# Performance work log

Hardware: AMD Instinct MI355X
Metric: run time of the kernel (lower is better)

## Reference

```python
import jax, jax.numpy as jnp
import numpy as np

B, S, E, H, M, Q = 2, 2048, 768, 12, 768, 4
D = E // H  # head_dim = 64
EPS = 1e-5


def _layernorm(x, g, b):
    m = jnp.mean(x, axis=-1, keepdims=True)
    v = jnp.mean((x - m) ** 2, axis=-1, keepdims=True)
    return (x - m) / jnp.sqrt(v + EPS) * g + b


def setup_inputs() -> dict:
    key = jax.random.key(0)
    ks = jax.random.split(key, 12)
    w = lambda k, shape, s=0.02: (jax.random.normal(k, shape) * s).astype(jnp.float32)
    return {
        "x": jax.random.normal(ks[0], (B, S, E), dtype=jnp.float32),
        "ln1_g": jnp.ones((E,), jnp.float32), "ln1_b": jnp.zeros((E,), jnp.float32),
        "wq": w(ks[1], (E, E)), "bq": jnp.zeros((E,), jnp.float32),
        "wk": w(ks[2], (E, E)), "bk": jnp.zeros((E,), jnp.float32),
        "wv": w(ks[3], (E, E)), "bv": jnp.zeros((E,), jnp.float32),
        "wo": w(ks[4], (E, E)), "bo": jnp.zeros((E,), jnp.float32),
        "ln2_g": jnp.ones((E,), jnp.float32), "ln2_b": jnp.zeros((E,), jnp.float32),
        "w1": w(ks[5], (E, Q * M)), "b1": jnp.zeros((Q * M,), jnp.float32),
        "wvqc": w(ks[6], (M, M)), "bvqc": jnp.zeros((M,), jnp.float32),
        "w2": w(ks[7], (Q * M, E)), "b2": jnp.zeros((E,), jnp.float32),
    }


def reference(x, ln1_g, ln1_b, wq, bq, wk, bk, wv, bv, wo, bo,
              ln2_g, ln2_b, w1, b1, wvqc, bvqc, w2, b2):
    b, s, e = x.shape
    h, d = H, e // H

    # --- attention branch (pre-norm, per-query-L2-normalized logits) ---
    xn = _layernorm(x, ln1_g, ln1_b)
    q = (xn @ wq + bq).reshape(b, s, h, d).transpose(0, 2, 1, 3)  # bhsd
    k = (xn @ wk + bk).reshape(b, s, h, d).transpose(0, 2, 1, 3)
    v = (xn @ wv + bv).reshape(b, s, h, d).transpose(0, 2, 1, 3)

    qk = jnp.einsum('bhsd,bhtd->bhst', q, k)                       # [B,H,S,S]
    q_norm2 = jnp.clip(jnp.sum(q * q, axis=-1, keepdims=True), 1e-5)  # [B,H,S,1]
    logits = qk / jnp.sqrt(d * q_norm2)
    attn = jax.nn.softmax(logits, axis=-1)
    vals = jnp.einsum('bhst,bhtd->bhsd', attn, v)
    vals = vals.transpose(0, 2, 1, 3).reshape(b, s, e)
    x = x + (vals @ wo + bo)  # residual; attn dropout is identity in eval

    # --- quantum-style FeedForward with overlapping q_stride slices ---
    xn2 = _layernorm(x, ln2_g, ln2_b)
    hmid = xn2 @ w1 + b1                                           # [B,S,Q*M]
    m = wvqc.shape[0]
    qstride = w1.shape[1] // m
    # overlapping slices h[..., i:i+M] for i in 0..Q-1, stacked on a new axis
    sl = jnp.stack([hmid[..., i:i + m] for i in range(qstride)], axis=2)  # [B,S,Q,M]
    hv = sl @ wvqc + bvqc                                          # vqc linear
    hv = hv.transpose(0, 1, 3, 2).reshape(b, s, qstride * m)       # interleave
    hv = jax.nn.gelu(hv, approximate=False)
    out = x + (hv @ w2 + b2)
    return out
```

## Files before the change

kernel.cpp:

```cpp
#include <hip/hip_runtime.h>
#include <hip/hip_bf16.h>
#include <math.h>

typedef unsigned short ushort_t;
typedef __attribute__((ext_vector_type(8))) short short8;
typedef __attribute__((ext_vector_type(8))) __bf16 bf16x8;
typedef __attribute__((ext_vector_type(4))) float f32x4;
typedef __attribute__((ext_vector_type(4))) unsigned u32x4;

#define SDIM 2048
#define EDIM 768
#define NTOK 4096

static __device__ __forceinline__ ushort_t f2bf(float f) {
  unsigned u = __builtin_bit_cast(unsigned, f);
  u += 0x7fff + ((u >> 16) & 1);
  return (ushort_t)(u >> 16);
}
static __device__ __forceinline__ float bf2f(ushort_t h) {
  return __builtin_bit_cast(float, (unsigned)h << 16);
}
static __device__ __forceinline__ f32x4 mfma16(short8 a, short8 b, f32x4 c) {
  return __builtin_amdgcn_mfma_f32_16x16x32_bf16(
      __builtin_bit_cast(bf16x8, a), __builtin_bit_cast(bf16x8, b), c, 0, 0, 0);
}
static __device__ __forceinline__ void gload_lds16(const void* g, void* l) {
  __builtin_amdgcn_global_load_lds(
      (const __attribute__((address_space(1))) void*)g,
      (__attribute__((address_space(3))) void*)l, 16, 0, 0);
}
static __device__ __forceinline__ unsigned cvtpk(float lo, float hi) {
  unsigned r;
  asm("v_cvt_pk_bf16_f32 %0, %1, %2" : "=v"(r) : "v"(lo), "v"(hi));
  return r;
}
static __device__ __forceinline__ float exp2fast(float x) {
  float r;
  asm("v_exp_f32 %0, %1" : "=v"(r) : "v"(x));
  return r;
}

__global__ void k_castT5(const float* __restrict__ wq, const float* __restrict__ wk,
                         const float* __restrict__ wv, const float* __restrict__ wo,
                         const float* __restrict__ wvqc, ushort_t* __restrict__ oqkv,
                         ushort_t* __restrict__ owo, ushort_t* __restrict__ ovqc) {
  __shared__ float tile[32][33];
  const int z = blockIdx.z;
  const float* in = z == 0 ? wq : z == 1 ? wk : z == 2 ? wv : z == 3 ? wo : wvqc;
  ushort_t* out = z < 3 ? oqkv + (size_t)z * 768 * 768 : (z == 3 ? owo : ovqc);
  int c0 = blockIdx.x * 32, r0 = blockIdx.y * 32;
  int tx = threadIdx.x, ty = threadIdx.y;
#pragma unroll
  for (int i = 0; i < 32; i += 8)
    tile[ty + i][tx] = in[(size_t)(r0 + ty + i) * 768 + c0 + tx];
  __syncthreads();
#pragma unroll
  for (int i = 0; i < 32; i += 8)
    out[(size_t)(c0 + ty + i) * 768 + r0 + tx] = f2bf(tile[tx][ty + i]);
}

__global__ void k_castT(const float* __restrict__ in, ushort_t* __restrict__ out,
                        int R, int C) {
  __shared__ float tile[32][33];
  int c0 = blockIdx.x * 32, r0 = blockIdx.y * 32;
  int tx = threadIdx.x, ty = threadIdx.y;
#pragma unroll
  for (int i = 0; i < 32; i += 8)
    tile[ty + i][tx] = in[(size_t)(r0 + ty + i) * C + c0 + tx];
  __syncthreads();
#pragma unroll
  for (int i = 0; i < 32; i += 8)
    out[(size_t)(c0 + ty + i) * R + r0 + tx] = f2bf(tile[tx][ty + i]);
}

__global__ void k_vT(const ushort_t* __restrict__ in, ushort_t* __restrict__ out) {
  __shared__ ushort_t tile[32][34];
  int bh = blockIdx.z;
  int t0 = blockIdx.x * 32, d0 = blockIdx.y * 32;
  const ushort_t* ib = in + (size_t)bh * SDIM * 64;
  ushort_t* ob = out + (size_t)bh * 64 * SDIM;
  int tx = threadIdx.x, ty = threadIdx.y;
#pragma unroll
  for (int i = 0; i < 32; i += 8)
    tile[ty + i][tx] = ib[(size_t)(t0 + ty + i) * 64 + d0 + tx];
  __syncthreads();
  const int T = t0 + tx, tb = T & ~63, tl = T & 63;
  const int tperm =
      tb + 32 * (tl >> 5) + 8 * ((tl >> 2) & 3) + 4 * ((tl >> 4) & 1) + (tl & 3);
#pragma unroll
  for (int i = 0; i < 32; i += 8)
    ob[(size_t)(d0 + ty + i) * SDIM + tperm] = tile[tx][ty + i];
}

__global__ void k_w1shift(const float* __restrict__ w1, ushort_t* __restrict__ w1s) {
  int idx = blockIdx.x * 256 + threadIdx.x;
  int e = idx / 768, m = idx - (idx / 768) * 768;
#pragma unroll
  for (int i = 0; i < 4; i++)
    w1s[((size_t)i * 768 + e) * 768 + m] = f2bf(w1[(size_t)e * 3072 + i + m]);
}

__global__ __launch_bounds__(256) void k_b1eff(const float* __restrict__ b1,
                                               const ushort_t* __restrict__ wvqcT,
                                               const float* __restrict__ bvqc,
                                               float* __restrict__ b1e) {
  const int n = blockIdx.x;
  const int i = n & 3, j = n >> 2;
  const int t = threadIdx.x;
  float s = 0.f;
  for (int m = t; m < 768; m += 256)
    s += b1[i + m] * bf2f(wvqcT[(size_t)j * 768 + m]);
#pragma unroll
  for (int mm = 32; mm; mm >>= 1) s += __shfl_xor(s, mm);
  __shared__ float red[4];
  if ((t & 63) == 0) red[t >> 6] = s;
  __syncthreads();
  if (t == 0) b1e[n] = red[0] + red[1] + red[2] + red[3] + bvqc[j];
}

__global__ __launch_bounds__(256) void k_ln(const float* __restrict__ x,
                                            const float* __restrict__ gam,
                                            const float* __restrict__ bet,
                                            ushort_t* __restrict__ out) {
  const int row = blockIdx.x, t = threadIdx.x;
  const float* xr = x + (size_t)row * EDIM;
  float v0 = xr[t], v1 = xr[t + 256], v2 = xr[t + 512];
  float s = v0 + v1 + v2;
  float s2 = v0 * v0 + v1 * v1 + v2 * v2;
#pragma unroll
  for (int m = 32; m; m >>= 1) { s += __shfl_xor(s, m); s2 += __shfl_xor(s2, m); }
  __shared__ float red[8];
  const int wid = t >> 6, lane = t & 63;
  if (lane == 0) { red[wid] = s; red[4 + wid] = s2; }
  __syncthreads();
  s = red[0] + red[1] + red[2] + red[3];
  s2 = red[4] + red[5] + red[6] + red[7];
  float mean = s * (1.f / EDIM);
  float var = s2 * (1.f / EDIM) - mean * mean;
  float rstd = rsqrtf(var + 1e-5f);
  ushort_t* orow = out + (size_t)row * EDIM;
  orow[t] = f2bf((v0 - mean) * rstd * gam[t] + bet[t]);
  orow[t + 256] = f2bf((v1 - mean) * rstd * gam[t + 256] + bet[t + 256]);
  orow[t + 512] = f2bf((v2 - mean) * rstd * gam[t + 512] + bet[t + 512]);
}

__global__ __launch_bounds__(256) void k_qscale(const ushort_t* __restrict__ q,
                                                float* __restrict__ qs) {
  const int lane = threadIdx.x & 63, w = threadIdx.x >> 6;
  const int row = blockIdx.x * 4 + w;
  float v = bf2f(q[(size_t)row * 64 + lane]);
  float s = v * v;
#pragma unroll
  for (int m = 32; m; m >>= 1) s += __shfl_xor(s, m);
  if (lane == 0) qs[row] = rsqrtf(64.f * fmaxf(s, 1e-5f));
}

template <int MODE, int BM, int BN, int BK>
__global__ __launch_bounds__(256) void k_gemm(
    const ushort_t* __restrict__ A, const ushort_t* __restrict__ Bt, int lda,
    int ldb, int kc, const float* __restrict__ b0, const float* __restrict__ b1p,
    const float* __restrict__ b2p, float* __restrict__ outF,
    const float* __restrict__ resid, ushort_t* __restrict__ o0,
    ushort_t* __restrict__ o1, ushort_t* __restrict__ o2, int ldc) {
  constexpr int MT = BM / 32, NT = BN / 32;
  constexpr int KCH = BK / 8;
  constexpr int NPA = BM * BK / 2048;
  constexpr int NPB = BN * BK / 2048;
  constexpr int ROWSP = 2048 / BK;
  constexpr int KK = BK / 32;
  __shared__ ushort_t As[2][BM * BK];
  __shared__ ushort_t Bs[2][BN * BK];
  const int t = threadIdx.x;
  const int m0 = blockIdx.x * BM, n0 = blockIdx.y * BN;
  if (MODE == 3) Bt += (size_t)blockIdx.z * 768 * 768;
  const int srow = t / KCH, sch = t % KCH;
  const int xs = (BK == 64) ? (srow & 7) : ((srow >> 1) & 3);
  const int gseg = (sch ^ xs) * 8;
  const ushort_t* ga = A + (size_t)(m0 + srow) * lda + gseg;
  const ushort_t* gb = Bt + (size_t)(n0 + srow) * ldb + gseg;
  const int ldst = t * 8;
  const int lane = t & 63, wid = t >> 6;
  const int g = lane >> 4, c = lane & 15;
  const int wm = (wid >> 1) * (BM / 2), wn = (wid & 1) * (BN / 2);
  const int xc = (BK == 64) ? (c & 7) : ((c >> 1) & 3);
  f32x4 acc[MT][NT] = {};

#define STAGE(BUF, K0)                                                           \
  {                                                                              \
    _Pragma("unroll") for (int p = 0; p < NPA; p++)                              \
        gload_lds16(ga + (K0) + (size_t)(p * ROWSP) * lda,                       \
                    As[BUF] + p * 2048 + ldst);                                  \
    _Pragma("unroll") for (int p = 0; p < NPB; p++)                              \
        gload_lds16(gb + (K0) + (size_t)(p * ROWSP) * ldb,                       \
                    Bs[BUF] + p * 2048 + ldst);                                  \
  }

  STAGE(0, 0);
  __syncthreads();
  int cur = 0;
  for (int k0 = 0; k0 < kc; k0 += BK) {
    if (k0 + BK < kc) STAGE(cur ^ 1, k0 + BK);
    short8 af[KK][MT], bfr[KK][NT];
#pragma unroll
    for (int kk = 0; kk < KK; kk++) {
#pragma unroll
      for (int mt = 0; mt < MT; mt++)
        af[kk][mt] = *(const short8*)(As[cur] + (wm + mt * 16 + c) * BK +
                                      (((g + kk * 4) ^ xc) * 8));
#pragma unroll
      for (int nt = 0; nt < NT; nt++)
        bfr[kk][nt] = *(const short8*)(Bs[cur] + (wn + nt * 16 + c) * BK +
                                       (((g + kk * 4) ^ xc) * 8));
    }
    __builtin_amdgcn_s_setprio(1);
#pragma unroll
    for (int kk = 0; kk < KK; kk++)
#pragma unroll
      for (int mt = 0; mt < MT; mt++)
#pragma unroll
        for (int nt = 0; nt < NT; nt++)
          acc[mt][nt] = mfma16(af[kk][mt], bfr[kk][nt], acc[mt][nt]);
    __builtin_amdgcn_s_setprio(0);
    __syncthreads();
    cur ^= 1;
  }
#undef STAGE

#pragma unroll
  for (int mt = 0; mt < MT; mt++) {
#pragma unroll
    for (int nt = 0; nt < NT; nt++) {
#pragma unroll
      for (int r = 0; r < 4; r++) {
        int row = m0 + wm + mt * 16 + g * 4 + r;
        int col = n0 + wn + nt * 16 + c;
        float val = acc[mt][nt][r];
        if constexpr (MODE == 0) {
          int which = col / 768;
          int nn = col - which * 768;
          int h = nn >> 6, d = nn & 63;
          int bb = row >> 11, s = row & 2047;
          const float* bp = which == 0 ? b0 : (which == 1 ? b1p : b2p);
          ushort_t* dp = which == 0 ? o0 : (which == 1 ? o1 : o2);
          dp[(((size_t)(bb * 12 + h)) * SDIM + s) * 64 + d] = f2bf(val + bp[nn]);
        } else if constexpr (MODE == 1) {
          size_t o = (size_t)row * ldc + col;
          outF[o] = resid[o] + val + b0[col];
        } else if constexpr (MODE == 2) {
          float xg = val + b0[col];
          float z2 = xg * (1.5957691216f + 0.0713548162f * xg * xg);
          float ge = xg / (1.f + __expf(-z2));
          o0[(size_t)row * ldc + col] = f2bf(ge);
        } else {
          o0[((size_t)row * 4 + blockIdx.z) * ldc + col] = f2bf(val);
        }
      }
    }
  }
}

__global__ __launch_bounds__(256) void k_attn(
    const ushort_t* __restrict__ q, const ushort_t* __restrict__ k,
    const ushort_t* __restrict__ vt, const float* __restrict__ qs,
    ushort_t* __restrict__ o0p, ushort_t* __restrict__ o1p,
    float* __restrict__ lpart) {
  const int tid = threadIdx.x;
  const int wid = tid >> 6, lane = tid & 63;
  const int g = lane >> 4, c = lane & 15;
  const int bh = blockIdx.y;
  const int z = blockIdx.z;
  const int tbase = z * (SDIM / 2);
  const int q0 = blockIdx.x * 64 + wid * 16;
  const int bb = bh / 12, h = bh - bb * 12;
  const ushort_t* qb = q + (size_t)bh * SDIM * 64;
  const ushort_t* kb = k + (size_t)bh * SDIM * 64;
  const ushort_t* vb = vt + (size_t)bh * 64 * SDIM;

  __shared__ ushort_t Ks[2][64 * 64];
  __shared__ ushort_t Vs[2][64 * 64];

  const float scq = qs[bh * SDIM + q0 + c] * 1.44269504089f;
  short8 a0 = *(const short8*)(qb + (size_t)(q0 + c) * 64 + g * 8);
  short8 a1 = *(const short8*)(qb + (size_t)(q0 + c) * 64 + 32 + g * 8);
  short8 bq0, bq1;
#pragma unroll
  for (int j = 0; j < 8; j++) {
    bq0[j] = (short)f2bf(bf2f((ushort_t)a0[j]) * scq);
    bq1[j] = (short)f2bf(bf2f((ushort_t)a1[j]) * scq);
  }
  const short8 ones = {0x3F80, 0x3F80, 0x3F80, 0x3F80,
                       0x3F80, 0x3F80, 0x3F80, 0x3F80};

  const int srow = tid >> 3, sj = tid & 7;

#define STAGE(BUF, T0)                                                          \
  {                                                                             \
    _Pragma("unroll") for (int n = 0; n < 2; n++) {                             \
      const int row = n * 32 + srow;                                            \
      const int scol = (sj ^ (row & 7)) * 8;                                    \
      gload_lds16(kb + (size_t)((T0) + row) * 64 + scol,                        \
                  Ks[BUF] + n * 2048 + tid * 8);                                \
      gload_lds16(vb + (size_t)row * SDIM + (T0) + scol,                        \
                  Vs[BUF] + n * 2048 + tid * 8);                                \
    }                                                                           \
  }

  f32x4 accO[4] = {};
  f32x4 accL = {};
  const int sw = (c & 7) << 4;

  STAGE(0, tbase);
  __syncthreads();
  int cur = 0;
  for (int tt = 0; tt < SDIM / 128; tt++) {
    const int t0 = tbase + tt * 64;
    if (tt + 1 < SDIM / 128) STAGE(cur ^ 1, t0 + 64);
    const char* Kc = (const char*)Ks[cur];
    const char* Vc = (const char*)Vs[cur];
    f32x4 s[4] = {};
    __builtin_amdgcn_s_setprio(1);
#pragma unroll
    for (int i = 0; i < 4; i++) {
      const int rb = (i * 16 + c) * 128;
      short8 ka0 = *(const short8*)(Kc + rb + ((g * 16) ^ sw));
      short8 ka1 = *(const short8*)(Kc + rb + ((64 + g * 16) ^ sw));
      s[i] = mfma16(ka0, bq0, s[i]);
      s[i] = mfma16(ka1, bq1, s[i]);
    }
    __builtin_amdgcn_s_setprio(0);
    short8 v0s[4], v1s[4];
#pragma unroll
    for (int dt = 0; dt < 4; dt++) {
      const int vbse = (dt * 16 + c) * 128;
      v0s[dt] = *(const short8*)(Vc + vbse + ((g * 16) ^ sw));
      v1s[dt] = *(const short8*)(Vc + vbse + ((64 + g * 16) ^ sw));
    }
    u32x4 w0 = {cvtpk(exp2fast(s[0][0]), exp2fast(s[0][1])),
                cvtpk(exp2fast(s[0][2]), exp2fast(s[0][3])),
                cvtpk(exp2fast(s[1][0]), exp2fast(s[1][1])),
                cvtpk(exp2fast(s[1][2]), exp2fast(s[1][3]))};
    u32x4 w1 = {cvtpk(exp2fast(s[2][0]), exp2fast(s[2][1])),
                cvtpk(exp2fast(s[2][2]), exp2fast(s[2][3])),
                cvtpk(exp2fast(s[3][0]), exp2fast(s[3][1])),
                cvtpk(exp2fast(s[3][2]), exp2fast(s[3][3]))};
    short8 pa0 = __builtin_bit_cast(short8, w0);
    short8 pa1 = __builtin_bit_cast(short8, w1);
    __builtin_amdgcn_s_setprio(1);
    accL = mfma16(pa0, ones, accL);
    accL = mfma16(pa1, ones, accL);
#pragma unroll
    for (int dt = 0; dt < 4; dt++) {
      accO[dt] = mfma16(pa0, v0s[dt], accO[dt]);
      accO[dt] = mfma16(pa1, v1s[dt], accO[dt]);
    }
    __builtin_amdgcn_s_setprio(0);
    __syncthreads();
    cur ^= 1;
  }
#undef STAGE

  if (c == 0) {
#pragma unroll
    for (int r = 0; r < 4; r++)
      lpart[((size_t)z * 24 + bh) * SDIM + q0 + 4 * g + r] = accL[r];
  }
  ushort_t* op = z ? o1p : o0p;
#pragma unroll
  for (int dt = 0; dt < 4; dt++)
#pragma unroll
    for (int r = 0; r < 4; r++) {
      int s = q0 + 4 * g + r;
      op[((size_t)(bb * SDIM + s)) * EDIM + h * 64 + dt * 16 + c] =
          f2bf(accO[dt][r]);
    }
}

__global__ __launch_bounds__(256) void k_comb(const ushort_t* __restrict__ o0p,
                                              const ushort_t* __restrict__ o1p,
                                              const float* __restrict__ lpart,
                                              ushort_t* __restrict__ vals) {
  const int gid = blockIdx.x * 256 + threadIdx.x;
  const int tok = gid / 96, ch = gid - tok * 96;
  const int h = ch >> 3;
  const int bb = tok >> 11, s = tok & 2047;
  const size_t lrow = (size_t)(bb * 12 + h) * SDIM + s;
  const float inv = 1.f / (lpart[lrow] + lpart[(size_t)24 * SDIM + lrow]);
  short8 a = *(const short8*)(o0p + (size_t)gid * 8);
  short8 b = *(const short8*)(o1p + (size_t)gid * 8);
  short8 o;
#pragma unroll
  for (int j = 0; j < 8; j++)
    o[j] = (short)f2bf((bf2f((ushort_t)a[j]) + bf2f((ushort_t)b[j])) * inv);
  *(short8*)(vals + (size_t)gid * 8) = o;
}

extern "C" void kernel_launch(void* const* d_in, const int* in_sizes, int n_in,
                              void* d_out, int out_size, void* d_ws, size_t ws_size,
                              hipStream_t stream) {
  const float* x = (const float*)d_in[0];
  const float* ln1g = (const float*)d_in[1];
  const float* ln1b = (const float*)d_in[2];
  const float* wq = (const float*)d_in[3];
  const float* bq = (const float*)d_in[4];
  const float* wk = (const float*)d_in[5];
  const float* bk = (const float*)d_in[6];
  const float* wv = (const float*)d_in[7];
  const float* bv = (const float*)d_in[8];
  const float* wo = (const float*)d_in[9];
  const float* bo = (const float*)d_in[10];
  const float* ln2g = (const float*)d_in[11];
  const float* ln2b = (const float*)d_in[12];
  const float* w1 = (const float*)d_in[13];
  const float* b1 = (const float*)d_in[14];
  const float* wvqc = (const float*)d_in[15];
  const float* bvqc = (const float*)d_in[16];
  const float* w2 = (const float*)d_in[17];
  const float* b2 = (const float*)d_in[18];
  float* out = (float*)d_out;

  char* w = (char*)d_ws;
  ushort_t* xn = (ushort_t*)(w + 0);
  ushort_t* vtb = (ushort_t*)(w + 0);
  ushort_t* xn2 = (ushort_t*)(w + 6291456);
  ushort_t* opart1 = (ushort_t*)(w + 6291456);
  float* x2 = (float*)(w + 12582912);
  ushort_t* qb = (ushort_t*)(w + 25165824);
  ushort_t* kb = (ushort_t*)(w + 31457280);
  ushort_t* vb = (ushort_t*)(w + 37748736);
  ushort_t* vals = (ushort_t*)(w + 44040192);
  ushort_t* G = (ushort_t*)(w + 25165824);
  float* qsc = (float*)(w + 50331648);
  ushort_t* wqkvT = (ushort_t*)(w + 50528256);
  ushort_t* woT = (ushort_t*)(w + 54067200);
  ushort_t* wvqcT = (ushort_t*)(w + 55246848);
  ushort_t* w1s = (ushort_t*)(w + 56426496);
  float* lpart = (float*)(w + 56426496);
  ushort_t* W1eT = (ushort_t*)(w + 61145088);
  float* b1e = (float*)(w + 65863680);
  ushort_t* w2T = (ushort_t*)(w + 65875968);

  dim3 tb(32, 8);
  k_castT5<<<dim3(24, 24, 5), tb, 0, stream>>>(wq, wk, wv, wo, wvqc, wqkvT, woT,
                                               wvqcT);
  k_castT<<<dim3(24, 96), tb, 0, stream>>>(w2, w2T, 3072, 768);
  k_w1shift<<<2304, 256, 0, stream>>>(w1, w1s);
  k_b1eff<<<3072, 256, 0, stream>>>(b1, wvqcT, bvqc, b1e);
  k_gemm<3, 128, 128, 32><<<dim3(6, 6, 4), 256, 0, stream>>>(
      wvqcT, w1s, 768, 768, 768, nullptr, nullptr, nullptr, nullptr, nullptr,
      W1eT, nullptr, nullptr, 768);
  k_ln<<<4096, 256, 0, stream>>>(x, ln1g, ln1b, xn);
  k_gemm<0, 128, 128, 32><<<dim3(32, 18), 256, 0, stream>>>(
      xn, wqkvT, 768, 768, 768, bq, bk, bv, nullptr, nullptr, qb, kb, vb, 0);
  k_vT<<<dim3(64, 2, 24), tb, 0, stream>>>(vb, vtb);
  k_qscale<<<12288, 256, 0, stream>>>(qb, qsc);
  k_attn<<<dim3(32, 24, 2), 256, 0, stream>>>(qb, kb, vtb, qsc, vals, opart1,
                                              lpart);
  k_comb<<<1536, 256, 0, stream>>>(vals, opart1, lpart, vals);
  k_gemm<1, 64, 64, 64><<<dim3(64, 12), 256, 0, stream>>>(
      vals, woT, 768, 768, 768, bo, nullptr, nullptr, x2, x, nullptr, nullptr,
      nullptr, 768);
  k_ln<<<4096, 256, 0, stream>>>(x2, ln2g, ln2b, xn2);
  k_gemm<2, 128, 128, 32><<<dim3(32, 24), 256, 0, stream>>>(
      xn2, W1eT, 768, 768, 768, b1e, nullptr, nullptr, nullptr, nullptr, G,
      nullptr, nullptr, 3072);
  k_gemm<1, 64, 64, 64><<<dim3(64, 12), 256, 0, stream>>>(
      G, w2T, 3072, 3072, 3072, b2, nullptr, nullptr, out, x2, nullptr, nullptr,
      nullptr, 768);
}
```

Before: 212.0 us.

## Process two query groups per wave in attention and split-K the final FFN GEMM

```diff
diff --git a/kernel.cpp b/kernel.cpp
--- a/kernel.cpp
+++ b/kernel.cpp
@@ -3,6 +3,7 @@
 #include <math.h>
 
 typedef unsigned short ushort_t;
+typedef __attribute__((ext_vector_type(4))) short s16x4;
 typedef __attribute__((ext_vector_type(8))) short short8;
 typedef __attribute__((ext_vector_type(8))) __bf16 bf16x8;
 typedef __attribute__((ext_vector_type(4))) float f32x4;
@@ -173,11 +174,12 @@
   const int t = threadIdx.x;
   const int m0 = blockIdx.x * BM, n0 = blockIdx.y * BN;
   if (MODE == 3) Bt += (size_t)blockIdx.z * 768 * 768;
+  const int koff = (MODE == 5) ? blockIdx.z * kc : 0;
   const int srow = t / KCH, sch = t % KCH;
   const int xs = (BK == 64) ? (srow & 7) : ((srow >> 1) & 3);
   const int gseg = (sch ^ xs) * 8;
-  const ushort_t* ga = A + (size_t)(m0 + srow) * lda + gseg;
-  const ushort_t* gb = Bt + (size_t)(n0 + srow) * ldb + gseg;
+  const ushort_t* ga = A + (size_t)(m0 + srow) * lda + koff + gseg;
+  const ushort_t* gb = Bt + (size_t)(n0 + srow) * ldb + koff + gseg;
   const int ldst = t * 8;
   const int lane = t & 63, wid = t >> 6;
   const int g = lane >> 4, c = lane & 15;
@@ -251,6 +253,9 @@
           float z2 = xg * (1.5957691216f + 0.0713548162f * xg * xg);
           float ge = xg / (1.f + __expf(-z2));
           o0[(size_t)row * ldc + col] = f2bf(ge);
+        } else if constexpr (MODE == 5) {
+          o0[(size_t)blockIdx.z * (NTOK * 768) + (size_t)row * ldc + col] =
+              f2bf(val);
         } else {
           o0[((size_t)row * 4 + blockIdx.z) * ldc + col] = f2bf(val);
         }
@@ -270,7 +275,7 @@
   const int bh = blockIdx.y;
   const int z = blockIdx.z;
   const int tbase = z * (SDIM / 2);
-  const int q0 = blockIdx.x * 64 + wid * 16;
+  const int q0 = blockIdx.x * 128 + wid * 32;
   const int bb = bh / 12, h = bh - bb * 12;
   const ushort_t* qb = q + (size_t)bh * SDIM * 64;
   const ushort_t* kb = k + (size_t)bh * SDIM * 64;
@@ -279,14 +284,18 @@
   __shared__ ushort_t Ks[2][64 * 64];
   __shared__ ushort_t Vs[2][64 * 64];
 
-  const float scq = qs[bh * SDIM + q0 + c] * 1.44269504089f;
-  short8 a0 = *(const short8*)(qb + (size_t)(q0 + c) * 64 + g * 8);
-  short8 a1 = *(const short8*)(qb + (size_t)(q0 + c) * 64 + 32 + g * 8);
-  short8 bq0, bq1;
-#pragma unroll
-  for (int j = 0; j < 8; j++) {
-    bq0[j] = (short)f2bf(bf2f((ushort_t)a0[j]) * scq);
-    bq1[j] = (short)f2bf(bf2f((ushort_t)a1[j]) * scq);
+  short8 bq[2][2];
+#pragma unroll
+  for (int qg = 0; qg < 2; qg++) {
+    const float scq = qs[bh * SDIM + q0 + qg * 16 + c] * 1.44269504089f;
+    short8 a0 = *(const short8*)(qb + (size_t)(q0 + qg * 16 + c) * 64 + g * 8);
+    short8 a1 =
+        *(const short8*)(qb + (size_t)(q0 + qg * 16 + c) * 64 + 32 + g * 8);
+#pragma unroll
+    for (int j = 0; j < 8; j++) {
+      bq[qg][0][j] = (short)f2bf(bf2f((ushort_t)a0[j]) * scq);
+      bq[qg][1][j] = (short)f2bf(bf2f((ushort_t)a1[j]) * scq);
+    }
   }
   const short8 ones = {0x3F80, 0x3F80, 0x3F80, 0x3F80,
                        0x3F80, 0x3F80, 0x3F80, 0x3F80};
@@ -305,8 +314,8 @@
     }                                                                           \
   }
 
-  f32x4 accO[4] = {};
-  f32x4 accL = {};
+  f32x4 accO[2][4] = {};
+  f32x4 accL[2] = {};
   const int sw = (c & 7) << 4;
 
   STAGE(0, tbase);
@@ -317,41 +326,53 @@
     if (tt + 1 < SDIM / 128) STAGE(cur ^ 1, t0 + 64);
     const char* Kc = (const char*)Ks[cur];
     const char* Vc = (const char*)Vs[cur];
-    f32x4 s[4] = {};
+    f32x4 s0[4] = {}, s1[4] = {};
     __builtin_amdgcn_s_setprio(1);
 #pragma unroll
     for (int i = 0; i < 4; i++) {
       const int rb = (i * 16 + c) * 128;
       short8 ka0 = *(const short8*)(Kc + rb + ((g * 16) ^ sw));
       short8 ka1 = *(const short8*)(Kc + rb + ((64 + g * 16) ^ sw));
-      s[i] = mfma16(ka0, bq0, s[i]);
-      s[i] = mfma16(ka1, bq1, s[i]);
+      s0[i] = mfma16(ka0, bq[0][0], s0[i]);
+      s1[i] = mfma16(ka0, bq[1][0], s1[i]);
+      s0[i] = mfma16(ka1, bq[0][1], s0[i]);
+      s1[i] = mfma16(ka1, bq[1][1], s1[i]);
     }
     __builtin_amdgcn_s_setprio(0);
-    short8 v0s[4], v1s[4];
+    u32x4 w00 = {cvtpk(exp2fast(s0[0][0]), exp2fast(s0[0][1])),
+                 cvtpk(exp2fast(s0[0][2]), exp2fast(s0[0][3])),
+                 cvtpk(exp2fast(s0[1][0]), exp2fast(s0[1][1])),
+                 cvtpk(exp2fast(s0[1][2]), exp2fast(s0[1][3]))};
+    u32x4 w10 = {cvtpk(exp2fast(s1[0][0]), exp2fast(s1[0][1])),
+                 cvtpk(exp2fast(s1[0][2]), exp2fast(s1[0][3])),
+                 cvtpk(exp2fast(s1[1][0]), exp2fast(s1[1][1])),
+                 cvtpk(exp2fast(s1[1][2]), exp2fast(s1[1][3]))};
+    u32x4 w01 = {cvtpk(exp2fast(s0[2][0]), exp2fast(s0[2][1])),
+                 cvtpk(exp2fast(s0[2][2]), exp2fast(s0[2][3])),
+                 cvtpk(exp2fast(s0[3][0]), exp2fast(s0[3][1])),
+                 cvtpk(exp2fast(s0[3][2]), exp2fast(s0[3][3]))};
+    u32x4 w11 = {cvtpk(exp2fast(s1[2][0]), exp2fast(s1[2][1])),
+                 cvtpk(exp2fast(s1[2][2]), exp2fast(s1[2][3])),
+                 cvtpk(exp2fast(s1[3][0]), exp2fast(s1[3][1])),
+                 cvtpk(exp2fast(s1[3][2]), exp2fast(s1[3][3]))};
+    short8 pa00 = __builtin_bit_cast(short8, w00);
+    short8 pa01 = __builtin_bit_cast(short8, w01);
+    short8 pa10 = __builtin_bit_cast(short8, w10);
+    short8 pa11 = __builtin_bit_cast(short8, w11);
+    __builtin_amdgcn_s_setprio(1);
+    accL[0] = mfma16(pa00, ones, accL[0]);
+    accL[1] = mfma16(pa10, ones, accL[1]);
+    accL[0] = mfma16(pa01, ones, accL[0]);
+    accL[1] = mfma16(pa11, ones, accL[1]);
 #pragma unroll
     for (int dt = 0; dt < 4; dt++) {
       const int vbse = (dt * 16 + c) * 128;
-      v0s[dt] = *(const short8*)(Vc + vbse + ((g * 16) ^ sw));
-      v1s[dt] = *(const short8*)(Vc + vbse + ((64 + g * 16) ^ sw));
-    }
-    u32x4 w0 = {cvtpk(exp2fast(s[0][0]), exp2fast(s[0][1])),
-                cvtpk(exp2fast(s[0][2]), exp2fast(s[0][3])),
-                cvtpk(exp2fast(s[1][0]), exp2fast(s[1][1])),
-                cvtpk(exp2fast(s[1][2]), exp2fast(s[1][3]))};
-    u32x4 w1 = {cvtpk(exp2fast(s[2][0]), exp2fast(s[2][1])),
-                cvtpk(exp2fast(s[2][2]), exp2fast(s[2][3])),
-                cvtpk(exp2fast(s[3][0]), exp2fast(s[3][1])),
-                cvtpk(exp2fast(s[3][2]), exp2fast(s[3][3]))};
-    short8 pa0 = __builtin_bit_cast(short8, w0);
-    short8 pa1 = __builtin_bit_cast(short8, w1);
-    __builtin_amdgcn_s_setprio(1);
-    accL = mfma16(pa0, ones, accL);
-    accL = mfma16(pa1, ones, accL);
-#pragma unroll
-    for (int dt = 0; dt < 4; dt++) {
-      accO[dt] = mfma16(pa0, v0s[dt], accO[dt]);
-      accO[dt] = mfma16(pa1, v1s[dt], accO[dt]);
+      short8 v0 = *(const short8*)(Vc + vbse + ((g * 16) ^ sw));
+      short8 v1 = *(const short8*)(Vc + vbse + ((64 + g * 16) ^ sw));
+      accO[0][dt] = mfma16(pa00, v0, accO[0][dt]);
+      accO[1][dt] = mfma16(pa10, v0, accO[1][dt]);
+      accO[0][dt] = mfma16(pa01, v1, accO[0][dt]);
+      accO[1][dt] = mfma16(pa11, v1, accO[1][dt]);
     }
     __builtin_amdgcn_s_setprio(0);
     __syncthreads();
@@ -359,20 +380,24 @@
   }
 #undef STAGE
 
-  if (c == 0) {
-#pragma unroll
-    for (int r = 0; r < 4; r++)
-      lpart[((size_t)z * 24 + bh) * SDIM + q0 + 4 * g + r] = accL[r];
-  }
   ushort_t* op = z ? o1p : o0p;
 #pragma unroll
-  for (int dt = 0; dt < 4; dt++)
-#pragma unroll
-    for (int r = 0; r < 4; r++) {
-      int s = q0 + 4 * g + r;
-      op[((size_t)(bb * SDIM + s)) * EDIM + h * 64 + dt * 16 + c] =
-          f2bf(accO[dt][r]);
+  for (int qg = 0; qg < 2; qg++) {
+    if (c == 0) {
+#pragma unroll
+      for (int r = 0; r < 4; r++)
+        lpart[((size_t)z * 24 + bh) * SDIM + q0 + qg * 16 + 4 * g + r] =
+            accL[qg][r];
     }
+#pragma unroll
+    for (int dt = 0; dt < 4; dt++)
+#pragma unroll
+      for (int r = 0; r < 4; r++) {
+        int s = q0 + qg * 16 + 4 * g + r;
+        op[((size_t)(bb * SDIM + s)) * EDIM + h * 64 + dt * 16 + c] =
+            f2bf(accO[qg][dt][r]);
+      }
+  }
 }
 
 __global__ __launch_bounds__(256) void k_comb(const ushort_t* __restrict__ o0p,
@@ -392,6 +417,22 @@
   for (int j = 0; j < 8; j++)
     o[j] = (short)f2bf((bf2f((ushort_t)a[j]) + bf2f((ushort_t)b[j])) * inv);
   *(short8*)(vals + (size_t)gid * 8) = o;
+}
+
+__global__ __launch_bounds__(256) void k_fin(const float* __restrict__ x2,
+                                             const float* __restrict__ b2,
+                                             const ushort_t* __restrict__ p,
+                                             float* __restrict__ out) {
+  const int i = blockIdx.x * 256 + threadIdx.x;
+  f32x4 r = ((const f32x4*)x2)[i];
+  f32x4 b = ((const f32x4*)b2)[i % 192];
+  s16x4 a0 = ((const s16x4*)p)[i];
+  s16x4 a1 = ((const s16x4*)(p + (size_t)NTOK * 768))[i];
+  f32x4 o;
+#pragma unroll
+  for (int j = 0; j < 4; j++)
+    o[j] = r[j] + b[j] + bf2f((ushort_t)a0[j]) + bf2f((ushort_t)a1[j]);
+  ((f32x4*)out)[i] = o;
 }
 
 extern "C" void kernel_launch(void* const* d_in, const int* in_sizes, int n_in,
@@ -438,6 +479,7 @@
   ushort_t* W1eT = (ushort_t*)(w + 61145088);
   float* b1e = (float*)(w + 65863680);
   ushort_t* w2T = (ushort_t*)(w + 65875968);
+  ushort_t* mp = (ushort_t*)(w + 0);
 
   dim3 tb(32, 8);
   k_castT5<<<dim3(24, 24, 5), tb, 0, stream>>>(wq, wk, wv, wo, wvqc, wqkvT, woT,
@@ -453,7 +495,7 @@
       xn, wqkvT, 768, 768, 768, bq, bk, bv, nullptr, nullptr, qb, kb, vb, 0);
   k_vT<<<dim3(64, 2, 24), tb, 0, stream>>>(vb, vtb);
   k_qscale<<<12288, 256, 0, stream>>>(qb, qsc);
-  k_attn<<<dim3(32, 24, 2), 256, 0, stream>>>(qb, kb, vtb, qsc, vals, opart1,
+  k_attn<<<dim3(16, 24, 2), 256, 0, stream>>>(qb, kb, vtb, qsc, vals, opart1,
                                               lpart);
   k_comb<<<1536, 256, 0, stream>>>(vals, opart1, lpart, vals);
   k_gemm<1, 64, 64, 64><<<dim3(64, 12), 256, 0, stream>>>(
@@ -463,7 +505,8 @@
   k_gemm<2, 128, 128, 32><<<dim3(32, 24), 256, 0, stream>>>(
       xn2, W1eT, 768, 768, 768, b1e, nullptr, nullptr, nullptr, nullptr, G,
       nullptr, nullptr, 3072);
-  k_gemm<1, 64, 64, 64><<<dim3(64, 12), 256, 0, stream>>>(
-      G, w2T, 3072, 3072, 3072, b2, nullptr, nullptr, out, x2, nullptr, nullptr,
-      nullptr, 768);
-}
+  k_gemm<5, 64, 64, 64><<<dim3(64, 12, 2), 256, 0, stream>>>(
+      G, w2T, 3072, 3072, 1536, nullptr, nullptr, nullptr, nullptr, nullptr, mp,
+      nullptr, nullptr, 768);
+  k_fin<<<3072, 256, 0, stream>>>(x2, b2, mp, out);
+}
```

After: 212.1 us. Within noise of the previous version (+0.0%).
